# Kernel optimization log

Measured on AMD Instinct MI355X. Metric: run time of the kernel, lower is better.

## Reference

```python
import jax, jax.numpy as jnp
import numpy as np

Nc, Ns, Nt, d_h, BS = 64, 64, 64, 128, 16


def setup_inputs() -> dict:
    key = jax.random.key(0)
    k1, k2, k3, k4, k5 = jax.random.split(key, 5)
    Ac = (jax.random.uniform(k1, (Ns, Nc)) < 0.05).astype(jnp.float32)
    As = (jax.random.uniform(k2, (Ns, Ns)) < 0.05).astype(jnp.float32)
    # AA = As@As@Ac + As@Ac + Ac, then binarize (masked_fill(AA != 0, 1))
    AA = As @ As @ Ac + As @ Ac + Ac
    AA = (AA != 0).astype(jnp.float32)                 # [Ns, Nc]
    AA_mask = jnp.tile(AA, (Nt, Nt))                   # [Ns*Nt, Nc*Nt], == AA.repeat(Nt,Nt) in torch
    GCW = jax.random.normal(k3, (Ns * Nt, Nc * Nt), dtype=jnp.float32)
    GCB = jax.random.normal(k4, (Ns * Nt, d_h), dtype=jnp.float32)
    h = jax.random.normal(k5, (BS, Nc, Nt, d_h), dtype=jnp.float32)
    e = jnp.zeros((1,), jnp.float32)                   # unused in forward (kept for signature parity)
    return {"h": h, "e": e, "AA_mask": AA_mask, "GCW": GCW, "GCB": GCB}


def reference(h, e, AA_mask, GCW, GCB):
    bs = h.shape[0]
    # A = relu(AA.repeat(Nt,Nt) * GCW)  -- structured masked weight [Ns*Nt, Nc*Nt]
    A = jax.nn.relu(AA_mask * GCW)
    # h: [bs, Nc, Nt, d_h] -> [bs, Nt, Nc, d_h] -> [bs, Nt*Nc, d_h]
    x = jnp.transpose(h, (0, 2, 1, 3)).reshape(bs, Nt * Nc, d_h)
    # relu(A @ x + GCB): [bs, Ns*Nt, d_h]
    x = jax.nn.relu(jnp.einsum('ij,bjd->bid', A, x) + GCB)
    # [bs, Nt, Ns, d_h] -> [bs, Ns, Nt, d_h] (final torch reshape is a no-op)
    x = x.reshape(bs, Nt, Ns, d_h)
    x = jnp.transpose(x, (0, 2, 1, 3))
    return x
```

## Files before the change

kernel.cpp:

```cpp
#include <hip/hip_runtime.h>


#define NC 64
#define NS 64
#define NT 64
#define DH 128
#define BATCH 16
#define MDIM 4096
#define KDIM 4096
#define TM 128
#define TK 64

typedef __attribute__((ext_vector_type(8))) short short8;
typedef __attribute__((ext_vector_type(4))) float floatx4;

__device__ __forceinline__ unsigned short f2bf(float f) {
    union { float f; unsigned int i; } v; v.f = f;
    return (unsigned short)((v.i + 0x7fffu + ((v.i >> 16) & 1u)) >> 16);
}
__device__ __forceinline__ void async16(const void* g, void* l) {
    __builtin_amdgcn_global_load_lds(
        (const __attribute__((address_space(1))) void*)g,
        (__attribute__((address_space(3))) void*)l, 16, 0, 0);
}

__global__ __launch_bounds__(256)
void prep(const float* __restrict__ aam, const float* __restrict__ gcw,
          const float* __restrict__ hmat,
          unsigned short* __restrict__ Abf, unsigned short* __restrict__ XT)
{
    const int tid = threadIdx.x;
    if ((int)blockIdx.x < MDIM) {
        const int i = blockIdx.x;
        __shared__ float sm[64];
        if (tid < 64) sm[tid] = aam[(size_t)(i & 63) * KDIM + tid];
        __syncthreads();
        const size_t base = (size_t)i * KDIM + tid * 16;
        floatx4 w0 = *(const floatx4*)(gcw + base);
        floatx4 w1 = *(const floatx4*)(gcw + base + 4);
        floatx4 w2 = *(const floatx4*)(gcw + base + 8);
        floatx4 w3 = *(const floatx4*)(gcw + base + 12);
        const float* m = &sm[(tid & 3) * 16];
        short8 p0, p1;
#pragma unroll
        for (int e = 0; e < 4; ++e) {
            float v0 = m[e]      * w0[e]; v0 = v0 > 0.f ? v0 : 0.f;
            float v1 = m[e + 4]  * w1[e]; v1 = v1 > 0.f ? v1 : 0.f;
            float v2 = m[e + 8]  * w2[e]; v2 = v2 > 0.f ? v2 : 0.f;
            float v3 = m[e + 12] * w3[e]; v3 = v3 > 0.f ? v3 : 0.f;
            p0[e]     = (short)f2bf(v0);
            p0[e + 4] = (short)f2bf(v1);
            p1[e]     = (short)f2bf(v2);
            p1[e + 4] = (short)f2bf(v3);
        }
        *(short8*)(Abf + base)     = p0;
        *(short8*)(Abf + base + 8) = p1;
    } else {
        const int blk = blockIdx.x - MDIM;
        const int b = blk >> 6;
        const int t = blk & 63;
        const int c0 = (tid & 7) * 8;
        const int d0 = tid >> 3;
#pragma unroll
        for (int it = 0; it < 4; ++it) {
            const int d = d0 + it * 32;
            short8 p;
#pragma unroll
            for (int e = 0; e < 8; ++e) {
                float v = hmat[(((size_t)b * NC + (c0 + e)) * NT + t) * DH + d];
                p[e] = (short)f2bf(v);
            }
            *(short8*)(XT + ((size_t)(b * DH + d)) * KDIM + t * 64 + c0) = p;
        }
    }
}

__global__ __launch_bounds__(256, 2)
void gemm(const unsigned short* __restrict__ Abf,
          const unsigned short* __restrict__ XT,
          const float* __restrict__ gcb,
          float* __restrict__ out)
{
    __shared__ short sA[TM * TK];
    __shared__ short sX[TM * TK];

    const int tid = threadIdx.x;
    const int bid = blockIdx.x;
    const int mp  = (bid & 7) * 4 + (bid >> 7);
    const int b   = (bid >> 3) & 15;
    const int i0  = mp * TM;

    const int lane = tid & 63;
    const int w    = tid >> 6;
    const int wm = (w >> 1) * 64;
    const int wn = (w & 1) * 64;
    const int l15 = lane & 15;
    const int q   = lane >> 4;

    const int srow = lane >> 3;
    const int schk = lane & 7;

    floatx4 acc[4][4];
#pragma unroll
    for (int mi = 0; mi < 4; ++mi)
#pragma unroll
        for (int ni = 0; ni < 4; ++ni)
            acc[mi][ni] = (floatx4){0.f, 0.f, 0.f, 0.f};

    for (int k0 = 0; k0 < KDIM; k0 += TK) {
        __syncthreads();
#pragma unroll
        for (int is = 0; is < 4; ++is) {
            const int r  = w * 8 + is * 32 + srow;
            const int kk = k0 + ((schk ^ (r & 7)) << 3);
            async16(Abf + (size_t)(i0 + r) * KDIM + kk, &sA[(w * 8 + is * 32) * TK]);
            async16(XT  + (size_t)(b * DH + r) * KDIM + kk, &sX[(w * 8 + is * 32) * TK]);
        }
        __syncthreads();

#pragma unroll
        for (int h = 0; h < 2; ++h) {
            short8 af[4], bf[4];
#pragma unroll
            for (int mi = 0; mi < 4; ++mi) {
                const int row = wm + mi * 16 + l15;
                af[mi] = *(const short8*)&sA[row * TK + (((h * 4 + q) ^ (l15 & 7)) << 3)];
            }
#pragma unroll
            for (int ni = 0; ni < 4; ++ni) {
                const int row = wn + ni * 16 + l15;
                bf[ni] = *(const short8*)&sX[row * TK + (((h * 4 + q) ^ (l15 & 7)) << 3)];
            }
#pragma unroll
            for (int mi = 0; mi < 4; ++mi)
#pragma unroll
                for (int ni = 0; ni < 4; ++ni)
                    acc[mi][ni] = __builtin_amdgcn_mfma_f32_16x16x32_bf16(
                        af[mi], bf[ni], acc[mi][ni], 0, 0, 0);
        }
    }

#pragma unroll
    for (int mi = 0; mi < 4; ++mi) {
        const int ibase = i0 + wm + mi * 16 + q * 4;
#pragma unroll
        for (int ni = 0; ni < 4; ++ni) {
            const int d = wn + ni * 16 + l15;
#pragma unroll
            for (int r = 0; r < 4; ++r) {
                const int i = ibase + r;
                float v = acc[mi][ni][r] + gcb[(size_t)i * DH + d];
                v = v > 0.f ? v : 0.f;
                out[(((size_t)b * NS + (i & 63)) * NT + (i >> 6)) * DH + d] = v;
            }
        }
    }
}

#define APAD 40
#define XPAD 20
__global__ __launch_bounds__(256, 2)
void gcn_fused(const float* __restrict__ hmat, const float* __restrict__ aam,
               const float* __restrict__ gcw, const float* __restrict__ gcb,
               float* __restrict__ out)
{
    __shared__ short sA[TM * APAD];
    __shared__ unsigned int sX[DH * XPAD];
    const int tid = threadIdx.x;
    const int bid = blockIdx.x;
    const int mp  = (bid & 7) * 4 + (bid >> 7);
    const int b   = (bid >> 3) & 15;
    const int i0  = mp * TM;
    const int lane = tid & 63;
    const int wm = ((tid >> 6) >> 1) * 64;
    const int wn = ((tid >> 6) & 1) * 64;
    const int l15 = lane & 15;
    const int q   = lane >> 4;
    floatx4 acc[4][4];
#pragma unroll
    for (int mi = 0; mi < 4; ++mi)
#pragma unroll
        for (int ni = 0; ni < 4; ++ni) acc[mi][ni] = (floatx4){0.f,0.f,0.f,0.f};
    const int ar = tid >> 2, ac = (tid & 3) << 3;
    const int kp = tid >> 4, dg = (tid & 15) << 3;
    const int wkey = (tid & 3) << 2;
    for (int k0 = 0; k0 < KDIM; k0 += 32) {
        const size_t ga0 = (size_t)(i0 + ar) * KDIM + (k0 + ac);
        const size_t ga1 = ga0 + (size_t)64 * KDIM;
        floatx4 aa0a = *(const floatx4*)(aam + ga0), aa0b = *(const floatx4*)(aam + ga0 + 4);
        floatx4 ww0a = *(const floatx4*)(gcw + ga0), ww0b = *(const floatx4*)(gcw + ga0 + 4);
        floatx4 aa1a = *(const floatx4*)(aam + ga1), aa1b = *(const floatx4*)(aam + ga1 + 4);
        floatx4 ww1a = *(const floatx4*)(gcw + ga1), ww1b = *(const floatx4*)(gcw + ga1 + 4);
        const int jj = k0 + 2 * kp, tt = jj >> 6, cc = jj & 63;
        const size_t gx0 = ((size_t)(b * NC + cc) * NT + tt) * DH + dg;
        const size_t gx1 = gx0 + (size_t)NT * DH;
        floatx4 x0a = *(const floatx4*)(hmat + gx0), x0b = *(const floatx4*)(hmat + gx0 + 4);
        floatx4 x1a = *(const floatx4*)(hmat + gx1), x1b = *(const floatx4*)(hmat + gx1 + 4);
        __syncthreads();
        short8 p0, p1;
#pragma unroll
        for (int e = 0; e < 4; ++e) {
            float v0 = aa0a[e]*ww0a[e]; v0 = v0>0.f?v0:0.f;
            float v1 = aa0b[e]*ww0b[e]; v1 = v1>0.f?v1:0.f;
            float v2 = aa1a[e]*ww1a[e]; v2 = v2>0.f?v2:0.f;
            float v3 = aa1b[e]*ww1b[e]; v3 = v3>0.f?v3:0.f;
            p0[e] = (short)f2bf(v0); p0[e+4] = (short)f2bf(v1);
            p1[e] = (short)f2bf(v2); p1[e+4] = (short)f2bf(v3);
        }
        *(short8*)&sA[ar * APAD + ac] = p0;
        *(short8*)&sA[(ar + 64) * APAD + ac] = p1;
#pragma unroll
        for (int e = 0; e < 4; ++e) {
            unsigned int pka = (unsigned int)f2bf(x0a[e]) | ((unsigned int)f2bf(x1a[e]) << 16);
            unsigned int pkb = (unsigned int)f2bf(x0b[e]) | ((unsigned int)f2bf(x1b[e]) << 16);
            sX[(dg + e) * XPAD + (kp ^ wkey)] = pka;
            sX[(dg + e + 4) * XPAD + (kp ^ wkey)] = pkb;
        }
        __syncthreads();
        short8 afrag[4], bfrag[4];
#pragma unroll
        for (int mi = 0; mi < 4; ++mi)
            afrag[mi] = *(const short8*)&sA[(wm + mi * 16 + l15) * APAD + q * 8];
#pragma unroll
        for (int ni = 0; ni < 4; ++ni) {
            const int row = wn + ni * 16 + l15;
            const int col = (q * 4) ^ (((row >> 3) & 3) << 2);
            bfrag[ni] = *(const short8*)(sX + row * XPAD + col);
        }
#pragma unroll
        for (int mi = 0; mi < 4; ++mi)
#pragma unroll
            for (int ni = 0; ni < 4; ++ni)
                acc[mi][ni] = __builtin_amdgcn_mfma_f32_16x16x32_bf16(
                    afrag[mi], bfrag[ni], acc[mi][ni], 0, 0, 0);
    }
#pragma unroll
    for (int mi = 0; mi < 4; ++mi) {
        const int ibase = i0 + wm + mi * 16 + q * 4;
#pragma unroll
        for (int ni = 0; ni < 4; ++ni) {
            const int d = wn + ni * 16 + l15;
#pragma unroll
            for (int r = 0; r < 4; ++r) {
                const int i = ibase + r;
                float v = acc[mi][ni][r] + gcb[(size_t)i * DH + d];
                v = v > 0.f ? v : 0.f;
                out[(((size_t)b * NS + (i & 63)) * NT + (i >> 6)) * DH + d] = v;
            }
        }
    }
}

extern "C" void kernel_launch(void* const* d_in, const int* in_sizes, int n_in,
                              void* d_out, int out_size, void* d_ws, size_t ws_size,
                              hipStream_t stream) {
    const float* h   = (const float*)d_in[0];
    const float* aam = (const float*)d_in[2];
    const float* gcw = (const float*)d_in[3];
    const float* gcb = (const float*)d_in[4];
    float* out = (float*)d_out;

    const size_t A_BYTES  = (size_t)MDIM * KDIM * 2;
    const size_t XT_BYTES = (size_t)BATCH * DH * KDIM * 2;

    if (ws_size >= A_BYTES + XT_BYTES) {
        unsigned short* Abf = (unsigned short*)d_ws;
        unsigned short* XT  = (unsigned short*)((char*)d_ws + A_BYTES);
        prep<<<dim3(MDIM + BATCH * NT), 256, 0, stream>>>(aam, gcw, h, Abf, XT);
        gemm<<<dim3((MDIM / TM) * BATCH), 256, 0, stream>>>(Abf, XT, gcb, out);
    } else {
        gcn_fused<<<dim3((MDIM / TM) * BATCH), 256, 0, stream>>>(h, aam, gcw, gcb, out);
    }
}
```

Before: 250.0 us.

## Triple-buffer GEMM LDS stages with 512-thread 128x256 tiles spanning batches

Reworks the bf16 GEMM so each block computes a 128x256 output tile whose N dimension spans two batch items, using 8 waves instead of 4. A three-stage LDS ring of async global-to-LDS loads with a vmcnt wait replaces the two-barrier load-then-compute loop, so loads for later K tiles overlap with MFMA work on the current one. It also raises wave priority around the MFMA bursts. In exchange it uses much more LDS per block (about 147 KB), which may limit occupancy, and the grid shrinks from 512 to 256 blocks.

Measured after the change: 237.0 us. 1.06x faster.

```diff
diff --git a/kernel.cpp b/kernel.cpp
--- a/kernel.cpp
+++ b/kernel.cpp
@@ -10,6 +10,10 @@
 #define KDIM 4096
 #define TM 128
 #define TK 64
+#define BM 128
+#define BN 256
+#define BK 64
+#define NTILES (KDIM / BK)
 
 typedef __attribute__((ext_vector_type(8))) short short8;
 typedef __attribute__((ext_vector_type(4))) float floatx4;
@@ -75,30 +79,33 @@
     }
 }
 
-__global__ __launch_bounds__(256, 2)
+__global__ __launch_bounds__(512, 2)
 void gemm(const unsigned short* __restrict__ Abf,
           const unsigned short* __restrict__ XT,
           const float* __restrict__ gcb,
           float* __restrict__ out)
 {
-    __shared__ short sA[TM * TK];
-    __shared__ short sX[TM * TK];
+    __shared__ short lds[3][(BM + BN) * BK];
 
     const int tid = threadIdx.x;
     const int bid = blockIdx.x;
-    const int mp  = (bid & 7) * 4 + (bid >> 7);
-    const int b   = (bid >> 3) & 15;
-    const int i0  = mp * TM;
+    const int np  = bid & 7;
+    const int mp  = bid >> 3;
+    const int i0  = mp * BM;
+    const int n0  = np * BN;
 
     const int lane = tid & 63;
     const int w    = tid >> 6;
-    const int wm = (w >> 1) * 64;
-    const int wn = (w & 1) * 64;
-    const int l15 = lane & 15;
-    const int q   = lane >> 4;
+    const int wm   = (w >> 2) * 64;
+    const int wn   = (w & 3) * 64;
+    const int l15  = lane & 15;
+    const int q    = lane >> 4;
 
     const int srow = lane >> 3;
-    const int schk = lane & 7;
+    const int swz  = ((lane & 7) ^ srow) << 3;
+
+    const unsigned short* Ab = Abf + (size_t)i0 * KDIM + swz;
+    const unsigned short* Xb = XT  + (size_t)n0 * KDIM + swz;
 
     floatx4 acc[4][4];
 #pragma unroll
@@ -107,51 +114,77 @@
         for (int ni = 0; ni < 4; ++ni)
             acc[mi][ni] = (floatx4){0.f, 0.f, 0.f, 0.f};
 
-    for (int k0 = 0; k0 < KDIM; k0 += TK) {
-        __syncthreads();
-#pragma unroll
-        for (int is = 0; is < 4; ++is) {
-            const int r  = w * 8 + is * 32 + srow;
-            const int kk = k0 + ((schk ^ (r & 7)) << 3);
-            async16(Abf + (size_t)(i0 + r) * KDIM + kk, &sA[(w * 8 + is * 32) * TK]);
-            async16(XT  + (size_t)(b * DH + r) * KDIM + kk, &sX[(w * 8 + is * 32) * TK]);
-        }
-        __syncthreads();
-
+    auto stage = [&](int t, int b) {
+        const int k0 = t * BK;
+        short* dst = lds[b];
+#pragma unroll
+        for (int ii = 0; ii < 2; ++ii) {
+            const int r = ii * 64 + w * 8 + srow;
+            async16(Ab + (size_t)r * KDIM + k0, dst + (ii * 64 + w * 8) * BK);
+        }
+#pragma unroll
+        for (int ii = 0; ii < 4; ++ii) {
+            const int r = ii * 64 + w * 8 + srow;
+            async16(Xb + (size_t)r * KDIM + k0, dst + (BM + ii * 64 + w * 8) * BK);
+        }
+    };
+
+    auto compute = [&](int b) {
+        const short* sA = lds[b];
+        const short* sX = lds[b] + BM * BK;
 #pragma unroll
         for (int h = 0; h < 2; ++h) {
-            short8 af[4], bf[4];
-#pragma unroll
-            for (int mi = 0; mi < 4; ++mi) {
-                const int row = wm + mi * 16 + l15;
-                af[mi] = *(const short8*)&sA[row * TK + (((h * 4 + q) ^ (l15 & 7)) << 3)];
-            }
-#pragma unroll
-            for (int ni = 0; ni < 4; ++ni) {
-                const int row = wn + ni * 16 + l15;
-                bf[ni] = *(const short8*)&sX[row * TK + (((h * 4 + q) ^ (l15 & 7)) << 3)];
-            }
+            const int co = ((h * 4 + q) ^ (l15 & 7)) << 3;
+            short8 af[4], xf[4];
+#pragma unroll
+            for (int mi = 0; mi < 4; ++mi)
+                af[mi] = *(const short8*)&sA[(wm + mi * 16 + l15) * BK + co];
+#pragma unroll
+            for (int ni = 0; ni < 4; ++ni)
+                xf[ni] = *(const short8*)&sX[(wn + ni * 16 + l15) * BK + co];
+            __builtin_amdgcn_s_setprio(1);
 #pragma unroll
             for (int mi = 0; mi < 4; ++mi)
 #pragma unroll
                 for (int ni = 0; ni < 4; ++ni)
                     acc[mi][ni] = __builtin_amdgcn_mfma_f32_16x16x32_bf16(
-                        af[mi], bf[ni], acc[mi][ni], 0, 0, 0);
-        }
-    }
+                        af[mi], xf[ni], acc[mi][ni], 0, 0, 0);
+            __builtin_amdgcn_s_setprio(0);
+        }
+    };
+
+    stage(0, 0);
+    stage(1, 1);
+
+    int bc = 0;
+    for (int t = 0; t < NTILES - 1; ++t) {
+        asm volatile("s_waitcnt vmcnt(6)" ::: "memory");
+        __builtin_amdgcn_s_barrier();
+        asm volatile("" ::: "memory");
+        int bs = bc + 2; if (bs >= 3) bs -= 3;
+        if (t + 2 < NTILES) stage(t + 2, bs);
+        compute(bc);
+        if (++bc == 3) bc = 0;
+    }
+    asm volatile("s_waitcnt vmcnt(0)" ::: "memory");
+    __builtin_amdgcn_s_barrier();
+    asm volatile("" ::: "memory");
+    compute(bc);
 
 #pragma unroll
     for (int mi = 0; mi < 4; ++mi) {
         const int ibase = i0 + wm + mi * 16 + q * 4;
 #pragma unroll
         for (int ni = 0; ni < 4; ++ni) {
-            const int d = wn + ni * 16 + l15;
+            const int n  = n0 + wn + ni * 16 + l15;
+            const int bb = n >> 7;
+            const int d  = n & 127;
 #pragma unroll
             for (int r = 0; r < 4; ++r) {
                 const int i = ibase + r;
                 float v = acc[mi][ni][r] + gcb[(size_t)i * DH + d];
                 v = v > 0.f ? v : 0.f;
-                out[(((size_t)b * NS + (i & 63)) * NT + (i >> 6)) * DH + d] = v;
+                out[(((size_t)bb * NS + (i & 63)) * NT + (i >> 6)) * DH + d] = v;
             }
         }
     }
@@ -267,7 +300,7 @@
         unsigned short* Abf = (unsigned short*)d_ws;
         unsigned short* XT  = (unsigned short*)((char*)d_ws + A_BYTES);
         prep<<<dim3(MDIM + BATCH * NT), 256, 0, stream>>>(aam, gcw, h, Abf, XT);
-        gemm<<<dim3((MDIM / TM) * BATCH), 256, 0, stream>>>(Abf, XT, gcb, out);
+        gemm<<<dim3((MDIM / BM) * (BATCH * DH / BN)), 512, 0, stream>>>(Abf, XT, gcb, out);
     } else {
         gcn_fused<<<dim3((MDIM / TM) * BATCH), 256, 0, stream>>>(h, aam, gcw, gcb, out);
     }
```
